# Kernel tuning notes

Hardware: AMD Instinct MI355X
Metric: run time of the kernel (lower is better)

## Reference

```python
import jax, jax.numpy as jnp
import numpy as np

PATCH = 3      # patch_size = (3, 3)
STRIDE = 1     # filter_patch_stride == compare_stride == 1
EPS = 1e-12    # F.normalize eps


def extract_patches(x, ph, pw, stride):
    """x: (B, C, H, W) -> (B, nH*nW, C, ph, pw), valid patches."""
    B, C, H, W = x.shape
    oh = (H - ph) // stride + 1
    ow = (W - pw) // stride + 1
    rows = (jnp.arange(oh) * stride)[:, None] + jnp.arange(ph)[None, :]  # (oh, ph)
    cols = (jnp.arange(ow) * stride)[:, None] + jnp.arange(pw)[None, :]  # (ow, pw)
    # gather -> (B, C, oh, ph, ow, pw)
    p = x[:, :, rows[:, :, None, None], cols[None, None, :, :]]
    return p.transpose(0, 2, 4, 1, 3, 5).reshape(B, oh * ow, C, ph, pw)


def l2norm(x, axis):
    # matches F.normalize(p=2): x / max(||x||, eps)
    return x / jnp.maximum(jnp.linalg.norm(x, axis=axis, keepdims=True), EPS)


def setup_inputs() -> dict:
    key = jax.random.key(0)
    k1, k2 = jax.random.split(key)
    pred_style = jax.random.normal(k1, (4, 256, 64, 64), dtype=jnp.float32)
    target_style = jax.random.normal(k2, (4, 256, 64, 64), dtype=jnp.float32)
    return {"pred_style": pred_style, "target_style": target_style}


def reference(pred_style, target_style):
    # patches of the raw (unnormalized) features
    tp = extract_patches(target_style, PATCH, PATCH, STRIDE)   # (B, nP, C, ph, pw)
    pp = extract_patches(pred_style, PATCH, PATCH, STRIDE)     # (B, nP, C, ph, pw)

    # best_match: normalize content feature over channels, style patches over channel dim (dim=2)
    x1n = l2norm(pred_style, axis=1)
    tpn = l2norm(tp, axis=2)
    x1p = extract_patches(x1n, PATCH, PATCH, STRIDE)           # (B, nP, C, ph, pw)

    # conv-as-cosine-correlation == batched patch dot products, then argmax over style patches
    scores = jnp.einsum('bqcij,bpcij->bqp', x1p, tpn)          # (B, nP, nP)
    match = jnp.argmax(scores, axis=2)                         # (B, nP)

    # gather best-matching target patches (indices detached in original via .data)
    new_t = jnp.take_along_axis(tp, match[:, :, None, None, None], axis=1)
    return jnp.mean((pp - new_t) ** 2)
```

## Files before the change

kernel.cpp:

```cpp
#include <hip/hip_runtime.h>
#include <hip/hip_bf16.h>

#define NB 4
#define CH 256
#define HH 64
#define WW 64
#define NPIX 4096
#define OH 62
#define NPATCH 3844
#define KDIM 256
#define EPSN 1e-12f
#define VROW 68
#define SEG 8
#define PST 68

typedef __attribute__((ext_vector_type(8))) short short8;
typedef __attribute__((ext_vector_type(4))) float f32x4;

__device__ __forceinline__ float bf16_to_f32(unsigned short u) {
    return __uint_as_float((unsigned)u << 16);
}
__device__ __forceinline__ unsigned short f32_to_bf16(float f) {
    __hip_bfloat16 h = __float2bfloat16(f);
    return *(unsigned short*)&h;
}

__global__ __launch_bounds__(256) void k_prep(const float* __restrict__ pred,
                                              const float* __restrict__ tgt,
                                              __hip_bfloat16* __restrict__ Xn,
                                              __hip_bfloat16* __restrict__ Tn,
                                              float* __restrict__ ssP, float* __restrict__ invP,
                                              float* __restrict__ ssT, float* __restrict__ invT,
                                              unsigned long long* __restrict__ keys,
                                              float* __restrict__ out) {
    const int bz = blockIdx.y;
    const int b = bz >> 1, which = bz & 1;
    const float* src = (which ? tgt : pred) + (size_t)b * CH * NPIX;
    unsigned short* dst = (unsigned short*)((which ? Tn : Xn) + (size_t)b * NPIX * CH);
    float* ss_g  = (which ? ssT  : ssP)  + b * NPIX;
    float* inv_g = (which ? invT : invP) + b * NPIX;
    const int pix0 = blockIdx.x * 64;
    const int t = threadIdx.x, lane = t & 63, wv = t >> 6;

    int gid = (bz * 64 + blockIdx.x) * 256 + t;
    if (gid < NB * NPATCH) keys[gid] = 0ull;
    if (gid == 0) out[0] = 0.f;

    __shared__ unsigned short stage[CH][PST];
    __shared__ float partial[16][68];
    __shared__ float inv_s[64];

    const int cb = t >> 4, chk = t & 15;
    float ss0 = 0.f, ss1 = 0.f, ss2 = 0.f, ss3 = 0.f;
#pragma unroll
    for (int r = 0; r < 16; ++r) {
        int c = cb * 16 + r;
        float4 v = *(const float4*)&src[(size_t)c * NPIX + pix0 + chk * 4];
        ss0 += v.x * v.x; ss1 += v.y * v.y; ss2 += v.z * v.z; ss3 += v.w * v.w;
        ushort4 sv;
        sv.x = f32_to_bf16(v.x); sv.y = f32_to_bf16(v.y);
        sv.z = f32_to_bf16(v.z); sv.w = f32_to_bf16(v.w);
        *(ushort4*)&stage[c][chk * 4] = sv;
    }
    float4 pv; pv.x = ss0; pv.y = ss1; pv.z = ss2; pv.w = ss3;
    *(float4*)&partial[cb][chk * 4] = pv;
    __syncthreads();
    if (t < 64) {
        float ss = 0.f;
#pragma unroll
        for (int r = 0; r < 16; ++r) ss += partial[r][t];
        float inv = 1.f / fmaxf(sqrtf(ss), EPSN);
        ss_g[pix0 + t] = ss;
        inv_g[pix0 + t] = inv;
        inv_s[t] = inv;
    }
    __syncthreads();
    for (int p = wv; p < 64; p += 4) {
        float iv = inv_s[p];
#pragma unroll
        for (int cc = 0; cc < 4; ++cc) {
            int c = cc * 64 + lane;
            float v = bf16_to_f32(stage[c][p]) * iv;
            dst[(size_t)(pix0 + p) * CH + c] = f32_to_bf16(v);
        }
    }
}

__device__ __forceinline__ void gload_lds16(const void* g, void* l) {
    __builtin_amdgcn_global_load_lds(
        (const __attribute__((address_space(1))) void*)g,
        (__attribute__((address_space(3))) void*)l, 16, 0, 0);
}

__global__ __launch_bounds__(512) void k_gemm(const __hip_bfloat16* __restrict__ A,
                                              const __hip_bfloat16* __restrict__ Bm,
                                              unsigned short* __restrict__ Dout) {
    __shared__ short As[2][8192];
    __shared__ short Bs[2][8192];
    const int z = blockIdx.z;
    const int t = threadIdx.x;
    const int lane = t & 63, wv = t >> 6;
    const int wm = wv >> 1, wn = wv & 1;
    const int row0 = blockIdx.y * 128, col0 = blockIdx.x * 128;
    const short* Ag = (const short*)A + (size_t)z * NPIX * CH;
    const short* Bg = (const short*)Bm + (size_t)z * NPIX * CH;
    unsigned short* D = Dout + (size_t)z * NPIX * NPIX;

    const int srow = t >> 3;
    const int kce  = ((t & 7) ^ (srow & 7)) * 8;

    f32x4 acc[2][4] = {};

#define STAGE_K(buf, k0)                                                                  \
    do {                                                                                  \
        gload_lds16(Ag + (size_t)(row0 + srow) * KDIM + (k0) + kce,      &As[buf][wv * 512]);        \
        gload_lds16(Ag + (size_t)(row0 + 64 + srow) * KDIM + (k0) + kce, &As[buf][4096 + wv * 512]); \
        gload_lds16(Bg + (size_t)(col0 + srow) * KDIM + (k0) + kce,      &Bs[buf][wv * 512]);        \
        gload_lds16(Bg + (size_t)(col0 + 64 + srow) * KDIM + (k0) + kce, &Bs[buf][4096 + wv * 512]); \
    } while (0)

    STAGE_K(0, 0);

    const int rsel = lane & 15, kq = lane >> 4;
    const int rx = rsel & 7;
#pragma unroll
    for (int it = 0; it < 4; ++it) {
        __syncthreads();
        const int buf = it & 1;
        if (it < 3) STAGE_K(buf ^ 1, (it + 1) * 64);
#pragma unroll
        for (int s = 0; s < 2; ++s) {
            const int pk = (((s << 2) + kq) ^ rx) * 8;
            short8 a[2], bfr[4];
#pragma unroll
            for (int mi = 0; mi < 2; ++mi)
                a[mi] = *(const short8*)&As[buf][(wm * 32 + mi * 16 + rsel) * 64 + pk];
#pragma unroll
            for (int ni = 0; ni < 4; ++ni)
                bfr[ni] = *(const short8*)&Bs[buf][(wn * 64 + ni * 16 + rsel) * 64 + pk];
#pragma unroll
            for (int mi = 0; mi < 2; ++mi)
#pragma unroll
                for (int ni = 0; ni < 4; ++ni)
                    acc[mi][ni] = __builtin_amdgcn_mfma_f32_16x16x32_bf16(a[mi], bfr[ni], acc[mi][ni], 0, 0, 0);
        }
    }
#undef STAGE_K
    const int rbase = (lane >> 4) * 4, cbase = lane & 15;
#pragma unroll
    for (int mi = 0; mi < 2; ++mi) {
#pragma unroll
        for (int ni = 0; ni < 4; ++ni) {
            int r0 = row0 + wm * 32 + mi * 16 + rbase;
            int c  = col0 + wn * 64 + ni * 16 + cbase;
#pragma unroll
            for (int r = 0; r < 4; ++r)
                D[(size_t)(r0 + r) * NPIX + c] = f32_to_bf16(acc[mi][ni][r]);
        }
    }
}

__device__ __forceinline__ void load_tile16(const unsigned short* __restrict__ D,
                                            int row, int col, float* f) {
    const unsigned short* rp = D + (size_t)row * NPIX + col;
    uint4 u0 = *(const uint4*)rp;
    uint4 u1 = *(const uint4*)(rp + 8);
    const unsigned* w0 = (const unsigned*)&u0;
    const unsigned* w1 = (const unsigned*)&u1;
#pragma unroll
    for (int w = 0; w < 4; ++w) {
        f[2 * w]         = bf16_to_f32((unsigned short)w0[w]);
        f[2 * w + 1]     = bf16_to_f32((unsigned short)(w0[w] >> 16));
        f[8 + 2 * w]     = bf16_to_f32((unsigned short)w1[w]);
        f[8 + 2 * w + 1] = bf16_to_f32((unsigned short)(w1[w] >> 16));
    }
}

__global__ __launch_bounds__(256) void k_score(const unsigned short* __restrict__ Dbase,
                                               unsigned long long* __restrict__ keys) {
    const int z = blockIdx.z;
    const unsigned short* D = Dbase + (size_t)z * NPIX * NPIX;
    const int t = threadIdx.x;

    const int d = (int)blockIdx.x - 61;
    const int adg = d < 0 ? -d : d;
    const int len = 62 - adg;
    const int s0 = blockIdx.y * SEG;
    if (s0 >= len) return;
    const int steps = min(SEG, len - s0);
    const int qr0 = (d > 0 ? d : 0) + s0;
    const int pr0 = qr0 - d;

    __shared__ __align__(16) float V[64 * VROW];

    const int a = t >> 2, b0 = (t & 3) * 16;
    const int g = t >> 6, qc = t & 63;
    const int qcr = qc < OH ? qc : (OH - 1);
    const int pc0 = g * 16;
    const int kmax = (g == 3) ? 14 : 16;

    float A[16], B[16], C[16];
    load_tile16(D, (qr0 + 0) * 64 + a, (pr0 + 0) * 64 + b0, A);
    load_tile16(D, (qr0 + 1) * 64 + a, (pr0 + 1) * 64 + b0, B);

    for (int k = 0; k < steps; ++k) {
        load_tile16(D, (qr0 + k + 2) * 64 + a, (pr0 + k + 2) * 64 + b0, C);
        float v[16];
#pragma unroll
        for (int e = 0; e < 16; ++e) v[e] = A[e] + B[e] + C[e];
        if (k) __syncthreads();
#pragma unroll
        for (int e = 0; e < 16; e += 4)
            *(f32x4*)&V[a * VROW + b0 + e] = *(const f32x4*)&v[e];
        __syncthreads();

        float r0[16], r1[20], r2[20];
#pragma unroll
        for (int e = 0; e < 16; e += 4)
            *(f32x4*)&r0[e] = *(const f32x4*)&V[qcr * VROW + pc0 + e];
#pragma unroll
        for (int e = 0; e < 20; e += 4)
            *(f32x4*)&r1[e] = *(const f32x4*)&V[(qcr + 1) * VROW + pc0 + e];
#pragma unroll
        for (int e = 0; e < 20; e += 4)
            *(f32x4*)&r2[e] = *(const f32x4*)&V[(qcr + 2) * VROW + pc0 + e];
        float best = -1e30f; int bpc = 0;
#pragma unroll
        for (int kk = 0; kk < 16; ++kk) {
            float s = r0[kk] + r1[kk + 1] + r2[kk + 2];
            if (kk < kmax && s > best) { best = s; bpc = pc0 + kk; }
        }
        if (qc < OH) {
            unsigned u = __float_as_uint(best);
            u = (best >= 0.f) ? (u | 0x80000000u) : ~u;
            unsigned long long key = ((unsigned long long)u << 12)
                                   | (unsigned)((63 - (pr0 + k)) << 6)
                                   | (unsigned)(63 - bpc);
            atomicMax(&keys[(size_t)z * NPATCH + (qr0 + k) * OH + qc], key);
        }
#pragma unroll
        for (int e = 0; e < 16; ++e) { A[e] = B[e]; B[e] = C[e]; }
    }
}

__global__ void k_loss(const unsigned short* __restrict__ Dbase,
                       const unsigned long long* __restrict__ keys,
                       const float* __restrict__ ssPb, const float* __restrict__ invPb,
                       const float* __restrict__ ssTb, const float* __restrict__ invTb,
                       float* __restrict__ out) {
    const int z = blockIdx.y;
    const unsigned short* D = Dbase + (size_t)z * NPIX * NPIX;
    const float* ssP  = ssPb  + z * NPIX;
    const float* invP = invPb + z * NPIX;
    const float* ssT  = ssTb  + z * NPIX;
    const float* invT = invTb + z * NPIX;
    int q = blockIdx.x * 256 + threadIdx.x;
    float acc = 0.f;
    if (q < NPATCH) {
        int qr = q / OH, qc = q - qr * OH;
        int qpix = qr * WW + qc;
        unsigned long long key = keys[(size_t)z * NPATCH + q];
        int mpr = 63 - (int)((key >> 6) & 63);
        int mpc = 63 - (int)(key & 63);
        int mpix = mpr * WW + mpc;
#pragma unroll
        for (int i = 0; i < 3; ++i)
#pragma unroll
            for (int j = 0; j < 3; ++j) {
                int off = i * WW + j;
                int y = qpix + off, x = mpix + off;
                float Dv = bf16_to_f32(D[(size_t)y * NPIX + x]);
                float nP = ssP[y] * invP[y];
                float nT = ssT[x] * invT[x];
                acc += ssP[y] + ssT[x] - 2.f * Dv * nP * nT;
            }
    }
#pragma unroll
    for (int s = 32; s > 0; s >>= 1) acc += __shfl_down(acc, s, 64);
    if ((threadIdx.x & 63) == 0)
        atomicAdd(out, acc * (1.f / 35426304.f));
}

extern "C" void kernel_launch(void* const* d_in, const int* in_sizes, int n_in,
                              void* d_out, int out_size, void* d_ws, size_t ws_size,
                              hipStream_t stream) {
    const float* pred = (const float*)d_in[0];
    const float* tgt  = (const float*)d_in[1];
    char* ws = (char*)d_ws;
    unsigned short*     Dws  = (unsigned short*)(ws);
    __hip_bfloat16*     Xn   = (__hip_bfloat16*)(ws + 134217728);
    __hip_bfloat16*     Tn   = (__hip_bfloat16*)(ws + 142606336);
    float*              ssP  = (float*)(ws + 150994944);
    float*              invP = (float*)(ws + 151060480);
    float*              ssT  = (float*)(ws + 151126016);
    float*              invT = (float*)(ws + 151191552);
    unsigned long long* keys = (unsigned long long*)(ws + 151257088);

    k_prep<<<dim3(64, 8), 256, 0, stream>>>(pred, tgt, Xn, Tn, ssP, invP, ssT, invT,
                                            keys, (float*)d_out);
    k_gemm<<<dim3(32, 32, 4), 512, 0, stream>>>(Xn, Tn, Dws);
    k_score<<<dim3(123, 8, 4), 256, 0, stream>>>(Dws, keys);
    k_loss<<<dim3(16, 4), 256, 0, stream>>>(Dws, keys, ssP, invP, ssT, invT,
                                            (float*)d_out);
}
```

Before: 174.6 us.

## Restructure GEMM to 4 waves with 64x64 warp tiles and LDS-staged stores

The score GEMM drops from 8 waves to 4 waves per 128x128 block, so each wave computes a 64x64 sub-tile (4x4 MFMA accumulators). This raises register reuse per LDS fragment load. Both K-stages are prefetched up front, with explicit vmcnt waits and barriers. Block IDs are swizzled to improve L2 locality. The output tile goes through an XOR-swizzled LDS buffer so global writes become coalesced 16-byte stores instead of scattered 2-byte ones. In exchange, register pressure per thread rises and there are fewer waves to hide latency.

```diff
diff --git a/kernel.cpp b/kernel.cpp
--- a/kernel.cpp
+++ b/kernel.cpp
@@ -92,16 +92,22 @@
         (__attribute__((address_space(3))) void*)l, 16, 0, 0);
 }
 
-__global__ __launch_bounds__(512) void k_gemm(const __hip_bfloat16* __restrict__ A,
-                                              const __hip_bfloat16* __restrict__ Bm,
-                                              unsigned short* __restrict__ Dout) {
-    __shared__ short As[2][8192];
-    __shared__ short Bs[2][8192];
-    const int z = blockIdx.z;
+__global__ __launch_bounds__(256, 2) void k_gemm(const __hip_bfloat16* __restrict__ A,
+                                                 const __hip_bfloat16* __restrict__ Bm,
+                                                 unsigned short* __restrict__ Dout) {
+    __shared__ __align__(16) short smem[32768];
+#define ASOFF(buf) ((buf) * 8192)
+#define BSOFF(buf) (16384 + (buf) * 8192)
+
     const int t = threadIdx.x;
     const int lane = t & 63, wv = t >> 6;
     const int wm = wv >> 1, wn = wv & 1;
-    const int row0 = blockIdx.y * 128, col0 = blockIdx.x * 128;
+
+    const int bid = ((blockIdx.z << 5) + blockIdx.y) * 32 + blockIdx.x;
+    const int swz = ((bid & 7) << 9) + (bid >> 3);
+    const int z = swz >> 10, by = (swz >> 5) & 31, bx = swz & 31;
+
+    const int row0 = by * 128, col0 = bx * 128;
     const short* Ag = (const short*)A + (size_t)z * NPIX * CH;
     const short* Bg = (const short*)Bm + (size_t)z * NPIX * CH;
     unsigned short* D = Dout + (size_t)z * NPIX * NPIX;
@@ -109,55 +115,92 @@
     const int srow = t >> 3;
     const int kce  = ((t & 7) ^ (srow & 7)) * 8;
 
-    f32x4 acc[2][4] = {};
-
-#define STAGE_K(buf, k0)                                                                  \
-    do {                                                                                  \
-        gload_lds16(Ag + (size_t)(row0 + srow) * KDIM + (k0) + kce,      &As[buf][wv * 512]);        \
-        gload_lds16(Ag + (size_t)(row0 + 64 + srow) * KDIM + (k0) + kce, &As[buf][4096 + wv * 512]); \
-        gload_lds16(Bg + (size_t)(col0 + srow) * KDIM + (k0) + kce,      &Bs[buf][wv * 512]);        \
-        gload_lds16(Bg + (size_t)(col0 + 64 + srow) * KDIM + (k0) + kce, &Bs[buf][4096 + wv * 512]); \
+    f32x4 acc[4][4] = {};
+
+#define STAGE_K(buf, k0)                                                                   \
+    do {                                                                                   \
+        _Pragma("unroll")                                                                  \
+        for (int rr_ = 0; rr_ < 4; ++rr_)                                                  \
+            gload_lds16(Ag + (size_t)(row0 + rr_ * 32 + srow) * KDIM + (k0) + kce,         \
+                        &smem[ASOFF(buf) + rr_ * 2048 + wv * 512]);                        \
+        _Pragma("unroll")                                                                  \
+        for (int rr_ = 0; rr_ < 4; ++rr_)                                                  \
+            gload_lds16(Bg + (size_t)(col0 + rr_ * 32 + srow) * KDIM + (k0) + kce,         \
+                        &smem[BSOFF(buf) + rr_ * 2048 + wv * 512]);                        \
     } while (0)
-
-    STAGE_K(0, 0);
 
     const int rsel = lane & 15, kq = lane >> 4;
     const int rx = rsel & 7;
-#pragma unroll
-    for (int it = 0; it < 4; ++it) {
-        __syncthreads();
-        const int buf = it & 1;
-        if (it < 3) STAGE_K(buf ^ 1, (it + 1) * 64);
-#pragma unroll
-        for (int s = 0; s < 2; ++s) {
-            const int pk = (((s << 2) + kq) ^ rx) * 8;
-            short8 a[2], bfr[4];
-#pragma unroll
-            for (int mi = 0; mi < 2; ++mi)
-                a[mi] = *(const short8*)&As[buf][(wm * 32 + mi * 16 + rsel) * 64 + pk];
-#pragma unroll
-            for (int ni = 0; ni < 4; ++ni)
-                bfr[ni] = *(const short8*)&Bs[buf][(wn * 64 + ni * 16 + rsel) * 64 + pk];
-#pragma unroll
-            for (int mi = 0; mi < 2; ++mi)
-#pragma unroll
-                for (int ni = 0; ni < 4; ++ni)
-                    acc[mi][ni] = __builtin_amdgcn_mfma_f32_16x16x32_bf16(a[mi], bfr[ni], acc[mi][ni], 0, 0, 0);
+
+#define CONSUME(buf)                                                                       \
+    do {                                                                                   \
+        _Pragma("unroll")                                                                  \
+        for (int s = 0; s < 2; ++s) {                                                      \
+            const int pk = (((s << 2) + kq) ^ rx) * 8;                                     \
+            short8 a_[4], b_[4];                                                           \
+            _Pragma("unroll")                                                              \
+            for (int mi = 0; mi < 4; ++mi)                                                 \
+                a_[mi] = *(const short8*)&smem[ASOFF(buf) + (wm * 64 + mi * 16 + rsel) * 64 + pk]; \
+            _Pragma("unroll")                                                              \
+            for (int ni = 0; ni < 4; ++ni)                                                 \
+                b_[ni] = *(const short8*)&smem[BSOFF(buf) + (wn * 64 + ni * 16 + rsel) * 64 + pk]; \
+            _Pragma("unroll")                                                              \
+            for (int mi = 0; mi < 4; ++mi)                                                 \
+                _Pragma("unroll")                                                          \
+                for (int ni = 0; ni < 4; ++ni)                                             \
+                    acc[mi][ni] = __builtin_amdgcn_mfma_f32_16x16x32_bf16(a_[mi], b_[ni],  \
+                                                                          acc[mi][ni], 0, 0, 0); \
+        }                                                                                  \
+    } while (0)
+
+#define KITER(it, VMC)                                              \
+    do {                                                            \
+        asm volatile("s_waitcnt vmcnt(" #VMC ")" ::: "memory");     \
+        __builtin_amdgcn_sched_barrier(0);                          \
+        __builtin_amdgcn_s_barrier();                               \
+        __builtin_amdgcn_sched_barrier(0);                          \
+        CONSUME((it) & 1);                                          \
+        asm volatile("s_waitcnt lgkmcnt(0)" ::: "memory");          \
+        __builtin_amdgcn_sched_barrier(0);                          \
+        __builtin_amdgcn_s_barrier();                               \
+        __builtin_amdgcn_sched_barrier(0);                          \
+        if ((it) < 2) STAGE_K((it) & 1, ((it) + 2) * 64);           \
+    } while (0)
+
+    STAGE_K(0, 0);
+    STAGE_K(1, 64);
+    KITER(0, 8);
+    KITER(1, 8);
+    KITER(2, 8);
+    KITER(3, 0);
+#undef KITER
+#undef CONSUME
+#undef STAGE_K
+
+    const int rbase = (lane >> 4) * 4, cbase = lane & 15;
+    unsigned short* Cs = (unsigned short*)smem;
+#pragma unroll
+    for (int mi = 0; mi < 4; ++mi)
+#pragma unroll
+        for (int ni = 0; ni < 4; ++ni) {
+            int c = wn * 64 + ni * 16 + cbase;
+#pragma unroll
+            for (int r = 0; r < 4; ++r) {
+                int row = wm * 64 + mi * 16 + rbase + r;
+                int pc = (((c >> 3) ^ (row & 15)) * 8) + (c & 7);
+                Cs[row * 128 + pc] = f32_to_bf16(acc[mi][ni][r]);
+            }
         }
-    }
-#undef STAGE_K
-    const int rbase = (lane >> 4) * 4, cbase = lane & 15;
-#pragma unroll
-    for (int mi = 0; mi < 2; ++mi) {
-#pragma unroll
-        for (int ni = 0; ni < 4; ++ni) {
-            int r0 = row0 + wm * 32 + mi * 16 + rbase;
-            int c  = col0 + wn * 64 + ni * 16 + cbase;
-#pragma unroll
-            for (int r = 0; r < 4; ++r)
-                D[(size_t)(r0 + r) * NPIX + c] = f32_to_bf16(acc[mi][ni][r]);
-        }
-    }
+    __syncthreads();
+#pragma unroll
+    for (int rd = 0; rd < 8; ++rd) {
+        int rr = rd * 16 + (t >> 4);
+        int pc = ((t & 15) ^ (rr & 15)) * 8;
+        uint4 v = *(const uint4*)&Cs[rr * 128 + pc];
+        *(uint4*)&D[(size_t)(row0 + rr) * NPIX + col0 + (t & 15) * 8] = v;
+    }
+#undef ASOFF
+#undef BSOFF
 }
 
 __device__ __forceinline__ void load_tile16(const unsigned short* __restrict__ D,
@@ -298,7 +341,7 @@
 
     k_prep<<<dim3(64, 8), 256, 0, stream>>>(pred, tgt, Xn, Tn, ssP, invP, ssT, invT,
                                             keys, (float*)d_out);
-    k_gemm<<<dim3(32, 32, 4), 512, 0, stream>>>(Xn, Tn, Dws);
+    k_gemm<<<dim3(32, 32, 4), 256, 0, stream>>>(Xn, Tn, Dws);
     k_score<<<dim3(123, 8, 4), 256, 0, stream>>>(Dws, keys);
     k_loss<<<dim3(16, 4), 256, 0, stream>>>(Dws, keys, ssP, invP, ssT, invT,
                                             (float*)d_out);
```

After: 181.2 us. +3.8%, slower.
